# Performance work log

Measured on AMD Instinct MI355X. Metric: run time of the kernel, lower is better.

## Reference

```python
import jax, jax.numpy as jnp
import numpy as np

ALPHA = 0.25
GAMMA = 2.0
EPS = 1e-4

B, A, C, M = 4, 100000, 80, 32


def setup_inputs() -> dict:
    key = jax.random.key(0)
    k1, k2, k3, k4, k5, k6 = jax.random.split(key, 6)
    clsfs = jax.random.uniform(k1, (B, A, C), dtype=jnp.float32)
    rgrss = jax.random.normal(k2, (B, A, 4), dtype=jnp.float32)
    # anchors: random centers/sizes on a 512x512 image, converted to x1y1x2y2
    ctr = jax.random.uniform(k3, (A, 2), minval=32.0, maxval=480.0)
    wh = jax.random.uniform(k4, (A, 2), minval=16.0, maxval=256.0)
    anc = jnp.concatenate([ctr - 0.5 * wh, ctr + 0.5 * wh], axis=1)
    ancs = anc[None, :, :].astype(jnp.float32)
    # annotations: [x1,y1,x2,y2,label]; all valid labels in [0, C)
    gctr = jax.random.uniform(k5, (B, M, 2), minval=64.0, maxval=448.0)
    gwh = jax.random.uniform(k6, (B, M, 2), minval=24.0, maxval=200.0)
    lbl = jax.random.randint(jax.random.fold_in(key, 7), (B, M, 1), 0, C).astype(jnp.float32)
    annos = jnp.concatenate([gctr - 0.5 * gwh, gctr + 0.5 * gwh, lbl], axis=2).astype(jnp.float32)
    return {"clsfs": clsfs, "rgrss": rgrss, "ancs": ancs, "annos": annos}


def calc_iou(a, b):
    # a: [A,4], b: [M,4] -> [A,M]
    area_b = (b[:, 2] - b[:, 0]) * (b[:, 3] - b[:, 1])
    area_a = (a[:, 2] - a[:, 0]) * (a[:, 3] - a[:, 1])
    iw = jnp.clip(jnp.minimum(a[:, None, 2], b[None, :, 2]) - jnp.maximum(a[:, None, 0], b[None, :, 0]), 0.0)
    ih = jnp.clip(jnp.minimum(a[:, None, 3], b[None, :, 3]) - jnp.maximum(a[:, None, 1], b[None, :, 1]), 0.0)
    inter = iw * ih
    ua = jnp.clip(area_a[:, None] + area_b[None, :] - inter, 1e-8)
    return inter / ua


def _per_image(clsf, rgrs, anns, anc, ancw, anch, ancx, ancy):
    valid = anns[:, 4] != -1.0  # [M]
    has_anns = valid.any()
    ious = calc_iou(anc, anns[:, :4])  # [A,M]
    ious = jnp.where(valid[None, :], ious, -1.0)  # mask padded annotations
    maxiou = ious.max(axis=1)
    maxidx = ious.argmax(axis=1)
    assigned = anns[maxidx]  # [A,5]
    pos = maxiou >= 0.5
    posnum = pos.sum().astype(clsf.dtype)

    # classification targets: -1 ignore, 0 negative (<0.4), one-hot for pos
    clsf = jnp.clip(clsf, EPS, 1.0 - EPS)
    nc = clsf.shape[1]
    targets = jnp.full(clsf.shape, -1.0, dtype=clsf.dtype)
    targets = jnp.where((maxiou < 0.4)[:, None], 0.0, targets)
    onehot = jnp.arange(nc)[None, :] == assigned[:, 4].astype(jnp.int32)[:, None]
    targets = jnp.where(pos[:, None], jnp.where(onehot, 1.0, 0.0), targets)

    alpha = jnp.where(targets == 1.0, ALPHA, 1.0 - ALPHA)
    focal = alpha * jnp.where(targets == 1.0, 1.0 - clsf, clsf) ** GAMMA
    bce = -(targets * jnp.log(clsf) + (1.0 - targets) * jnp.log(1.0 - clsf))
    clsloss = jnp.where(targets != -1.0, focal * bce, 0.0).sum() / jnp.maximum(posnum, 1.0)

    gtw0 = assigned[:, 2] - assigned[:, 0]
    gth0 = assigned[:, 3] - assigned[:, 1]
    gtx = assigned[:, 0] + 0.5 * gtw0
    gty = assigned[:, 1] + 0.5 * gth0
    gtw = jnp.maximum(gtw0, 1.0)
    gth = jnp.maximum(gth0, 1.0)
    t = jnp.stack([(gtx - ancx) / ancw,
                   (gty - ancy) / anch,
                   jnp.log(gtw / ancw),
                   jnp.log(gth / anch)], axis=1)
    t = t / jnp.array([0.1, 0.1, 0.2, 0.2], dtype=clsf.dtype)
    diff = jnp.abs(t - rgrs)
    sl1 = jnp.where(diff <= 1.0 / 9.0, 0.5 * 9.0 * diff * diff, diff - 0.5 / 9.0)
    regloss = jnp.where(pos[:, None], sl1, 0.0).sum() / jnp.maximum(posnum * 4.0, 1.0)
    regloss = jnp.where(posnum > 0, regloss, 0.0)

    clsloss = jnp.where(has_anns, clsloss, 0.0)
    regloss = jnp.where(has_anns, regloss, 0.0)
    return clsloss, regloss


def reference(clsfs, rgrss, ancs, annos):
    anc = ancs[0]
    ancw = anc[:, 2] - anc[:, 0]
    anch = anc[:, 3] - anc[:, 1]
    ancx = anc[:, 0] + 0.5 * ancw
    ancy = anc[:, 1] + 0.5 * anch
    cls_l, reg_l = jax.vmap(_per_image, in_axes=(0, 0, 0, None, None, None, None, None))(
        clsfs, rgrss, annos, anc, ancw, anch, ancx, ancy)
    return cls_l.mean(keepdims=True), reg_l.mean(keepdims=True)
```

## Files before the change

kernel.cpp:

```cpp
#include <hip/hip_runtime.h>

#define F_EPS 1e-4f

constexpr int B = 4, A = 100000, C = 80, M = 32;
constexpr int APB = 256;
constexpr int THREADS = 256;
constexpr int VPA = C / 4;
constexpr int BPI = (A + APB - 1) / APB;
constexpr int FPT = APB * VPA / THREADS;

struct Part { float cls, reg, pos, pad; };

__device__ __forceinline__ float fterm(float p) {
  p = fminf(fmaxf(p, F_EPS), 1.0f - F_EPS);
  return p * p * (-__logf(1.0f - p));
}
__device__ __forceinline__ float fquad(float4 v) {
  return (fterm(v.x) + fterm(v.y)) + (fterm(v.z) + fterm(v.w));
}

__global__ __launch_bounds__(THREADS) void focal_main(
    const float* __restrict__ clsfs,
    const float* __restrict__ rgrss,
    const float* __restrict__ ancs,
    const float* __restrict__ annos,
    Part* __restrict__ part) {
  const int b = blockIdx.x / BPI;
  const int ablk = blockIdx.x - b * BPI;
  const int a0 = ablk * APB;
  const int tid = threadIdx.x;

  __shared__ float s_ann[M * 5];
  __shared__ float s_w[APB];
  __shared__ float s_red[3][THREADS / 64];

  if (tid < M * 5) s_ann[tid] = annos[b * M * 5 + tid];
  __syncthreads();

  float reg_acc = 0.0f, corr_acc = 0.0f, pos_acc = 0.0f;

  {
    const int a = a0 + tid;
    float wv = 0.0f;
    if (a < A) {
      const float4 anc = ((const float4*)ancs)[a];
      const float ax1 = anc.x, ay1 = anc.y, ax2 = anc.z, ay2 = anc.w;
      const float area_a = (ax2 - ax1) * (ay2 - ay1);
      float maxiou = -2.0f;
      int maxidx = 0;
      #pragma unroll
      for (int m = 0; m < M; ++m) {
        const float bx1 = s_ann[m * 5 + 0], by1 = s_ann[m * 5 + 1];
        const float bx2 = s_ann[m * 5 + 2], by2 = s_ann[m * 5 + 3];
        float iou = -1.0f;
        if (s_ann[m * 5 + 4] != -1.0f) {
          float iw = fmaxf(fminf(ax2, bx2) - fmaxf(ax1, bx1), 0.0f);
          float ih = fmaxf(fminf(ay2, by2) - fmaxf(ay1, by1), 0.0f);
          float inter = iw * ih;
          float area_b = (bx2 - bx1) * (by2 - by1);
          float ua = fmaxf(area_a + area_b - inter, 1e-8f);
          iou = inter / ua;
        }
        if (iou > maxiou) { maxiou = iou; maxidx = m; }
      }
      if (maxiou >= 0.5f) {
        const int lbl = (int)s_ann[maxidx * 5 + 4];
        pos_acc = 1.0f;
        wv = 1.0f;
        float p = clsfs[((size_t)b * A + a) * C + lbl];
        p = fminf(fmaxf(p, F_EPS), 1.0f - F_EPS);
        const float q = 1.0f - p;
        corr_acc = 0.25f * q * q * (-__logf(p)) - 0.75f * p * p * (-__logf(q));
        const float bx1 = s_ann[maxidx * 5 + 0], by1 = s_ann[maxidx * 5 + 1];
        const float bx2 = s_ann[maxidx * 5 + 2], by2 = s_ann[maxidx * 5 + 3];
        const float ancw = ax2 - ax1, anch = ay2 - ay1;
        const float ancx = ax1 + 0.5f * ancw, ancy = ay1 + 0.5f * anch;
        const float gtw0 = bx2 - bx1, gth0 = by2 - by1;
        const float gtx = bx1 + 0.5f * gtw0, gty = by1 + 0.5f * gth0;
        const float gtw = fmaxf(gtw0, 1.0f), gth = fmaxf(gth0, 1.0f);
        const float t0 = ((gtx - ancx) / ancw) / 0.1f;
        const float t1 = ((gty - ancy) / anch) / 0.1f;
        const float t2 = __logf(gtw / ancw) / 0.2f;
        const float t3 = __logf(gth / anch) / 0.2f;
        const float4 r = ((const float4*)rgrss)[(size_t)b * A + a];
        const float th = 1.0f / 9.0f, hh = 0.5f / 9.0f;
        float d;
        d = fabsf(t0 - r.x); reg_acc += (d <= th) ? 4.5f * d * d : d - hh;
        d = fabsf(t1 - r.y); reg_acc += (d <= th) ? 4.5f * d * d : d - hh;
        d = fabsf(t2 - r.z); reg_acc += (d <= th) ? 4.5f * d * d : d - hh;
        d = fabsf(t3 - r.w); reg_acc += (d <= th) ? 4.5f * d * d : d - hh;
      } else if (maxiou < 0.4f) {
        wv = 1.0f;
      }
    }
    s_w[tid] = wv;
  }
  __syncthreads();

  const int nanch = min(APB, A - a0);
  const float4* __restrict__ base4 =
      (const float4*)(clsfs + ((size_t)b * A + a0) * C);
  float acc0 = 0.f, acc1 = 0.f, acc2 = 0.f, acc3 = 0.f;
  if (nanch == APB) {
    #pragma unroll
    for (int k = 0; k < FPT; k += 4) {
      const int i0 = tid + (k + 0) * THREADS;
      const int i1 = tid + (k + 1) * THREADS;
      const int i2 = tid + (k + 2) * THREADS;
      const int i3 = tid + (k + 3) * THREADS;
      const float4 v0 = base4[i0];
      const float4 v1 = base4[i1];
      const float4 v2 = base4[i2];
      const float4 v3 = base4[i3];
      const float w0 = s_w[i0 / VPA];
      const float w1 = s_w[i1 / VPA];
      const float w2 = s_w[i2 / VPA];
      const float w3 = s_w[i3 / VPA];
      acc0 += w0 * fquad(v0);
      acc1 += w1 * fquad(v1);
      acc2 += w2 * fquad(v2);
      acc3 += w3 * fquad(v3);
    }
  } else {
    const int nvec = nanch * VPA;
    for (int i = tid; i < nvec; i += THREADS)
      acc0 += s_w[i / VPA] * fquad(base4[i]);
  }
  float cls_acc = 0.75f * ((acc0 + acc1) + (acc2 + acc3)) + corr_acc;

  float reg_f = reg_acc, pos_f = pos_acc;
  #pragma unroll
  for (int off = 32; off > 0; off >>= 1) {
    cls_acc += __shfl_down(cls_acc, off);
    reg_f   += __shfl_down(reg_f, off);
    pos_f   += __shfl_down(pos_f, off);
  }
  const int wave = tid >> 6, lane = tid & 63;
  if (lane == 0) { s_red[0][wave] = cls_acc; s_red[1][wave] = reg_f; s_red[2][wave] = pos_f; }
  __syncthreads();
  if (tid == 0) {
    float bc = 0.f, br = 0.f, bp = 0.f;
    #pragma unroll
    for (int v = 0; v < THREADS / 64; ++v) {
      bc += s_red[0][v]; br += s_red[1][v]; bp += s_red[2][v];
    }
    Part q; q.cls = bc; q.reg = br; q.pos = bp; q.pad = 0.f;
    part[blockIdx.x] = q;
  }
}

__global__ __launch_bounds__(256) void focal_final(
    const float* __restrict__ annos,
    const Part* __restrict__ part,
    float* __restrict__ out) {
  const int tid = threadIdx.x;
  const int wv = tid >> 6, lane = tid & 63;
  __shared__ float s_cls[4], s_reg[4];

  double c = 0.0, r = 0.0;
  float p = 0.f;
  for (int j = lane; j < BPI; j += 64) {
    const Part q = part[wv * BPI + j];
    c += (double)q.cls; r += (double)q.reg; p += q.pos;
  }
  #pragma unroll
  for (int off = 32; off > 0; off >>= 1) {
    c += __shfl_down(c, off);
    r += __shfl_down(r, off);
    p += __shfl_down(p, off);
  }
  const bool valid = (lane < M) && (annos[(wv * M + lane) * 5 + 4] != -1.0f);
  const bool has = __any(valid);
  if (lane == 0) {
    const float pn = p;
    float cls = (float)(c / (double)fmaxf(pn, 1.0f));
    float reg = (pn > 0.f) ? (float)(r / ((double)pn * 4.0)) : 0.0f;
    if (!has) { cls = 0.f; reg = 0.f; }
    s_cls[wv] = cls; s_reg[wv] = reg;
  }
  __syncthreads();
  if (tid == 0) {
    out[0] = (s_cls[0] + s_cls[1] + s_cls[2] + s_cls[3]) * 0.25f;
    out[1] = (s_reg[0] + s_reg[1] + s_reg[2] + s_reg[3]) * 0.25f;
  }
}

extern "C" void kernel_launch(void* const* d_in, const int* in_sizes, int n_in,
                              void* d_out, int out_size, void* d_ws, size_t ws_size,
                              hipStream_t stream) {
  const float* clsfs = (const float*)d_in[0];
  const float* rgrss = (const float*)d_in[1];
  const float* ancs  = (const float*)d_in[2];
  const float* annos = (const float*)d_in[3];
  float* out = (float*)d_out;
  Part* part = (Part*)d_ws;

  focal_main<<<dim3(B * BPI), dim3(THREADS), 0, stream>>>(
      clsfs, rgrss, ancs, annos, part);
  focal_final<<<1, 256, 0, stream>>>(annos, part, out);
}
```

Baseline: 42.45 us.

## Split anchor assignment and classification streaming into separate kernels

Anchor IoU matching now runs in its own kernel, which writes per-anchor negative weights to workspace. A separate grid-strided streaming kernel (512 blocks per image, 15-16 float4 loads per thread) reads the class scores. It uses log2 with the ln2 and 0.75 factors folded into the weight constant. This decouples the compute-heavy IoU phase from the bandwidth-bound sweep so the sweep can keep more loads in flight, at the cost of an extra launch and a weight-array round trip through memory.

```diff
diff --git a/kernel.cpp b/kernel.cpp
--- a/kernel.cpp
+++ b/kernel.cpp
@@ -3,155 +3,201 @@
 #define F_EPS 1e-4f
 
 constexpr int B = 4, A = 100000, C = 80, M = 32;
+constexpr int THREADS = 256;
 constexpr int APB = 256;
-constexpr int THREADS = 256;
+constexpr int BPI = (A + APB - 1) / APB;
 constexpr int VPA = C / 4;
-constexpr int BPI = (A + APB - 1) / APB;
-constexpr int FPT = APB * VPA / THREADS;
+constexpr int TVI = A * VPA;
+constexpr int SBX = 512;
+constexpr int SG = SBX * THREADS;
+constexpr float WNEG = -0.5198603854199589f;
 
 struct Part { float cls, reg, pos, pad; };
 
-__device__ __forceinline__ float fterm(float p) {
-  p = fminf(fmaxf(p, F_EPS), 1.0f - F_EPS);
-  return p * p * (-__logf(1.0f - p));
-}
-__device__ __forceinline__ float fquad(float4 v) {
-  return (fterm(v.x) + fterm(v.y)) + (fterm(v.z) + fterm(v.w));
-}
-
-__global__ __launch_bounds__(THREADS) void focal_main(
+__global__ __launch_bounds__(THREADS) void focal_assign(
     const float* __restrict__ clsfs,
     const float* __restrict__ rgrss,
     const float* __restrict__ ancs,
     const float* __restrict__ annos,
+    float* __restrict__ wn,
     Part* __restrict__ part) {
   const int b = blockIdx.x / BPI;
-  const int ablk = blockIdx.x - b * BPI;
-  const int a0 = ablk * APB;
+  const int a = (blockIdx.x - b * BPI) * APB + threadIdx.x;
   const int tid = threadIdx.x;
 
   __shared__ float s_ann[M * 5];
-  __shared__ float s_w[APB];
   __shared__ float s_red[3][THREADS / 64];
-
   if (tid < M * 5) s_ann[tid] = annos[b * M * 5 + tid];
   __syncthreads();
 
   float reg_acc = 0.0f, corr_acc = 0.0f, pos_acc = 0.0f;
 
-  {
-    const int a = a0 + tid;
+  if (a < A) {
     float wv = 0.0f;
-    if (a < A) {
-      const float4 anc = ((const float4*)ancs)[a];
-      const float ax1 = anc.x, ay1 = anc.y, ax2 = anc.z, ay2 = anc.w;
-      const float area_a = (ax2 - ax1) * (ay2 - ay1);
-      float maxiou = -2.0f;
-      int maxidx = 0;
-      #pragma unroll
-      for (int m = 0; m < M; ++m) {
-        const float bx1 = s_ann[m * 5 + 0], by1 = s_ann[m * 5 + 1];
-        const float bx2 = s_ann[m * 5 + 2], by2 = s_ann[m * 5 + 3];
-        float iou = -1.0f;
-        if (s_ann[m * 5 + 4] != -1.0f) {
-          float iw = fmaxf(fminf(ax2, bx2) - fmaxf(ax1, bx1), 0.0f);
-          float ih = fmaxf(fminf(ay2, by2) - fmaxf(ay1, by1), 0.0f);
-          float inter = iw * ih;
-          float area_b = (bx2 - bx1) * (by2 - by1);
-          float ua = fmaxf(area_a + area_b - inter, 1e-8f);
-          iou = inter / ua;
-        }
-        if (iou > maxiou) { maxiou = iou; maxidx = m; }
+    const float4 anc = ((const float4*)ancs)[a];
+    const float ax1 = anc.x, ay1 = anc.y, ax2 = anc.z, ay2 = anc.w;
+    const float area_a = (ax2 - ax1) * (ay2 - ay1);
+    float maxiou = -2.0f;
+    int maxidx = 0;
+    #pragma unroll
+    for (int m = 0; m < M; ++m) {
+      const float bx1 = s_ann[m * 5 + 0], by1 = s_ann[m * 5 + 1];
+      const float bx2 = s_ann[m * 5 + 2], by2 = s_ann[m * 5 + 3];
+      float iou = -1.0f;
+      if (s_ann[m * 5 + 4] != -1.0f) {
+        float iw = fmaxf(fminf(ax2, bx2) - fmaxf(ax1, bx1), 0.0f);
+        float ih = fmaxf(fminf(ay2, by2) - fmaxf(ay1, by1), 0.0f);
+        float inter = iw * ih;
+        float area_b = (bx2 - bx1) * (by2 - by1);
+        float ua = fmaxf(area_a + area_b - inter, 1e-8f);
+        iou = inter / ua;
       }
-      if (maxiou >= 0.5f) {
-        const int lbl = (int)s_ann[maxidx * 5 + 4];
-        pos_acc = 1.0f;
-        wv = 1.0f;
-        float p = clsfs[((size_t)b * A + a) * C + lbl];
-        p = fminf(fmaxf(p, F_EPS), 1.0f - F_EPS);
-        const float q = 1.0f - p;
-        corr_acc = 0.25f * q * q * (-__logf(p)) - 0.75f * p * p * (-__logf(q));
-        const float bx1 = s_ann[maxidx * 5 + 0], by1 = s_ann[maxidx * 5 + 1];
-        const float bx2 = s_ann[maxidx * 5 + 2], by2 = s_ann[maxidx * 5 + 3];
-        const float ancw = ax2 - ax1, anch = ay2 - ay1;
-        const float ancx = ax1 + 0.5f * ancw, ancy = ay1 + 0.5f * anch;
-        const float gtw0 = bx2 - bx1, gth0 = by2 - by1;
-        const float gtx = bx1 + 0.5f * gtw0, gty = by1 + 0.5f * gth0;
-        const float gtw = fmaxf(gtw0, 1.0f), gth = fmaxf(gth0, 1.0f);
-        const float t0 = ((gtx - ancx) / ancw) / 0.1f;
-        const float t1 = ((gty - ancy) / anch) / 0.1f;
-        const float t2 = __logf(gtw / ancw) / 0.2f;
-        const float t3 = __logf(gth / anch) / 0.2f;
-        const float4 r = ((const float4*)rgrss)[(size_t)b * A + a];
-        const float th = 1.0f / 9.0f, hh = 0.5f / 9.0f;
-        float d;
-        d = fabsf(t0 - r.x); reg_acc += (d <= th) ? 4.5f * d * d : d - hh;
-        d = fabsf(t1 - r.y); reg_acc += (d <= th) ? 4.5f * d * d : d - hh;
-        d = fabsf(t2 - r.z); reg_acc += (d <= th) ? 4.5f * d * d : d - hh;
-        d = fabsf(t3 - r.w); reg_acc += (d <= th) ? 4.5f * d * d : d - hh;
-      } else if (maxiou < 0.4f) {
-        wv = 1.0f;
-      }
+      if (iou > maxiou) { maxiou = iou; maxidx = m; }
     }
-    s_w[tid] = wv;
-  }
-  __syncthreads();
-
-  const int nanch = min(APB, A - a0);
-  const float4* __restrict__ base4 =
-      (const float4*)(clsfs + ((size_t)b * A + a0) * C);
-  float acc0 = 0.f, acc1 = 0.f, acc2 = 0.f, acc3 = 0.f;
-  if (nanch == APB) {
-    #pragma unroll
-    for (int k = 0; k < FPT; k += 4) {
-      const int i0 = tid + (k + 0) * THREADS;
-      const int i1 = tid + (k + 1) * THREADS;
-      const int i2 = tid + (k + 2) * THREADS;
-      const int i3 = tid + (k + 3) * THREADS;
-      const float4 v0 = base4[i0];
-      const float4 v1 = base4[i1];
-      const float4 v2 = base4[i2];
-      const float4 v3 = base4[i3];
-      const float w0 = s_w[i0 / VPA];
-      const float w1 = s_w[i1 / VPA];
-      const float w2 = s_w[i2 / VPA];
-      const float w3 = s_w[i3 / VPA];
-      acc0 += w0 * fquad(v0);
-      acc1 += w1 * fquad(v1);
-      acc2 += w2 * fquad(v2);
-      acc3 += w3 * fquad(v3);
+    if (maxiou >= 0.5f) {
+      const int lbl = (int)s_ann[maxidx * 5 + 4];
+      pos_acc = 1.0f;
+      wv = 1.0f;
+      float p = clsfs[((size_t)b * A + a) * C + lbl];
+      p = fminf(fmaxf(p, F_EPS), 1.0f - F_EPS);
+      const float q = 1.0f - p;
+      corr_acc = 0.25f * q * q * (-__logf(p)) - 0.75f * p * p * (-__logf(q));
+      const float bx1 = s_ann[maxidx * 5 + 0], by1 = s_ann[maxidx * 5 + 1];
+      const float bx2 = s_ann[maxidx * 5 + 2], by2 = s_ann[maxidx * 5 + 3];
+      const float ancw = ax2 - ax1, anch = ay2 - ay1;
+      const float ancx = ax1 + 0.5f * ancw, ancy = ay1 + 0.5f * anch;
+      const float gtw0 = bx2 - bx1, gth0 = by2 - by1;
+      const float gtx = bx1 + 0.5f * gtw0, gty = by1 + 0.5f * gth0;
+      const float gtw = fmaxf(gtw0, 1.0f), gth = fmaxf(gth0, 1.0f);
+      const float t0 = ((gtx - ancx) / ancw) / 0.1f;
+      const float t1 = ((gty - ancy) / anch) / 0.1f;
+      const float t2 = __logf(gtw / ancw) / 0.2f;
+      const float t3 = __logf(gth / anch) / 0.2f;
+      const float4 r = ((const float4*)rgrss)[(size_t)b * A + a];
+      const float th = 1.0f / 9.0f, hh = 0.5f / 9.0f;
+      float d;
+      d = fabsf(t0 - r.x); reg_acc += (d <= th) ? 4.5f * d * d : d - hh;
+      d = fabsf(t1 - r.y); reg_acc += (d <= th) ? 4.5f * d * d : d - hh;
+      d = fabsf(t2 - r.z); reg_acc += (d <= th) ? 4.5f * d * d : d - hh;
+      d = fabsf(t3 - r.w); reg_acc += (d <= th) ? 4.5f * d * d : d - hh;
+    } else if (maxiou < 0.4f) {
+      wv = 1.0f;
     }
-  } else {
-    const int nvec = nanch * VPA;
-    for (int i = tid; i < nvec; i += THREADS)
-      acc0 += s_w[i / VPA] * fquad(base4[i]);
-  }
-  float cls_acc = 0.75f * ((acc0 + acc1) + (acc2 + acc3)) + corr_acc;
-
-  float reg_f = reg_acc, pos_f = pos_acc;
+    wn[(size_t)b * A + a] = wv * WNEG;
+  }
+
+  float cls_f = corr_acc, reg_f = reg_acc, pos_f = pos_acc;
   #pragma unroll
   for (int off = 32; off > 0; off >>= 1) {
-    cls_acc += __shfl_down(cls_acc, off);
-    reg_f   += __shfl_down(reg_f, off);
-    pos_f   += __shfl_down(pos_f, off);
+    cls_f += __shfl_down(cls_f, off);
+    reg_f += __shfl_down(reg_f, off);
+    pos_f += __shfl_down(pos_f, off);
   }
   const int wave = tid >> 6, lane = tid & 63;
-  if (lane == 0) { s_red[0][wave] = cls_acc; s_red[1][wave] = reg_f; s_red[2][wave] = pos_f; }
+  if (lane == 0) { s_red[0][wave] = cls_f; s_red[1][wave] = reg_f; s_red[2][wave] = pos_f; }
   __syncthreads();
   if (tid == 0) {
     float bc = 0.f, br = 0.f, bp = 0.f;
     #pragma unroll
-    for (int v = 0; v < THREADS / 64; ++v) {
-      bc += s_red[0][v]; br += s_red[1][v]; bp += s_red[2][v];
-    }
+    for (int v = 0; v < THREADS / 64; ++v) { bc += s_red[0][v]; br += s_red[1][v]; bp += s_red[2][v]; }
     Part q; q.cls = bc; q.reg = br; q.pos = bp; q.pad = 0.f;
     part[blockIdx.x] = q;
+  }
+}
+
+__device__ __forceinline__ float gterm(float p) {
+  const float pc = fminf(fmaxf(p, F_EPS), 1.0f - F_EPS);
+  return pc * pc * __log2f(1.0f - pc);
+}
+__device__ __forceinline__ float gquad(float4 v) {
+  return (gterm(v.x) + gterm(v.y)) + (gterm(v.z) + gterm(v.w));
+}
+
+__global__ __launch_bounds__(THREADS) void focal_stream(
+    const float* __restrict__ clsfs,
+    const float* __restrict__ wn,
+    float* __restrict__ part2) {
+  const int b = blockIdx.y;
+  const float4* __restrict__ base = (const float4*)(clsfs + (size_t)b * A * C);
+  const float* __restrict__ w = wn + (size_t)b * A;
+  const int i0 = blockIdx.x * THREADS + threadIdx.x;
+
+  float a0 = 0.f, a1 = 0.f, a2 = 0.f, a3 = 0.f;
+
+  {
+    float4 v0 = base[i0];
+    float4 v1 = base[i0 + 1 * SG];
+    float4 v2 = base[i0 + 2 * SG];
+    float4 v3 = base[i0 + 3 * SG];
+    float4 v4 = base[i0 + 4 * SG];
+    float4 v5 = base[i0 + 5 * SG];
+    float4 v6 = base[i0 + 6 * SG];
+    float4 v7 = base[i0 + 7 * SG];
+    float w0 = w[(i0) / VPA];
+    float w1 = w[(i0 + 1 * SG) / VPA];
+    float w2 = w[(i0 + 2 * SG) / VPA];
+    float w3 = w[(i0 + 3 * SG) / VPA];
+    float w4 = w[(i0 + 4 * SG) / VPA];
+    float w5 = w[(i0 + 5 * SG) / VPA];
+    float w6 = w[(i0 + 6 * SG) / VPA];
+    float w7 = w[(i0 + 7 * SG) / VPA];
+    a0 += w0 * gquad(v0);
+    a1 += w1 * gquad(v1);
+    a2 += w2 * gquad(v2);
+    a3 += w3 * gquad(v3);
+    a0 += w4 * gquad(v4);
+    a1 += w5 * gquad(v5);
+    a2 += w6 * gquad(v6);
+    a3 += w7 * gquad(v7);
+  }
+  {
+    float4 v0 = base[i0 + 8 * SG];
+    float4 v1 = base[i0 + 9 * SG];
+    float4 v2 = base[i0 + 10 * SG];
+    float4 v3 = base[i0 + 11 * SG];
+    float4 v4 = base[i0 + 12 * SG];
+    float4 v5 = base[i0 + 13 * SG];
+    float4 v6 = base[i0 + 14 * SG];
+    float w0 = w[(i0 + 8 * SG) / VPA];
+    float w1 = w[(i0 + 9 * SG) / VPA];
+    float w2 = w[(i0 + 10 * SG) / VPA];
+    float w3 = w[(i0 + 11 * SG) / VPA];
+    float w4 = w[(i0 + 12 * SG) / VPA];
+    float w5 = w[(i0 + 13 * SG) / VPA];
+    float w6 = w[(i0 + 14 * SG) / VPA];
+    a0 += w0 * gquad(v0);
+    a1 += w1 * gquad(v1);
+    a2 += w2 * gquad(v2);
+    a3 += w3 * gquad(v3);
+    a0 += w4 * gquad(v4);
+    a1 += w5 * gquad(v5);
+    a2 += w6 * gquad(v6);
+  }
+  {
+    const int i = i0 + 15 * SG;
+    if (i < TVI) a3 += w[i / VPA] * gquad(base[i]);
+  }
+
+  float cls = (a0 + a1) + (a2 + a3);
+  #pragma unroll
+  for (int off = 32; off > 0; off >>= 1) cls += __shfl_down(cls, off);
+
+  __shared__ float s_red[THREADS / 64];
+  const int wave = threadIdx.x >> 6, lane = threadIdx.x & 63;
+  if (lane == 0) s_red[wave] = cls;
+  __syncthreads();
+  if (threadIdx.x == 0) {
+    float bc = 0.f;
+    #pragma unroll
+    for (int v = 0; v < THREADS / 64; ++v) bc += s_red[v];
+    part2[b * SBX + blockIdx.x] = bc;
   }
 }
 
 __global__ __launch_bounds__(256) void focal_final(
     const float* __restrict__ annos,
     const Part* __restrict__ part,
+    const float* __restrict__ part2,
     float* __restrict__ out) {
   const int tid = threadIdx.x;
   const int wv = tid >> 6, lane = tid & 63;
@@ -163,6 +209,7 @@
     const Part q = part[wv * BPI + j];
     c += (double)q.cls; r += (double)q.reg; p += q.pos;
   }
+  for (int j = lane; j < SBX; j += 64) c += (double)part2[wv * SBX + j];
   #pragma unroll
   for (int off = 32; off > 0; off >>= 1) {
     c += __shfl_down(c, off);
@@ -193,9 +240,13 @@
   const float* ancs  = (const float*)d_in[2];
   const float* annos = (const float*)d_in[3];
   float* out = (float*)d_out;
-  Part* part = (Part*)d_ws;
-
-  focal_main<<<dim3(B * BPI), dim3(THREADS), 0, stream>>>(
-      clsfs, rgrss, ancs, annos, part);
-  focal_final<<<1, 256, 0, stream>>>(annos, part, out);
-}
+
+  Part*  part  = (Part*)d_ws;
+  float* part2 = (float*)((char*)d_ws + 32768);
+  float* wn    = (float*)((char*)d_ws + 65536);
+
+  focal_assign<<<dim3(B * BPI), dim3(THREADS), 0, stream>>>(
+      clsfs, rgrss, ancs, annos, wn, part);
+  focal_stream<<<dim3(SBX, B), dim3(THREADS), 0, stream>>>(clsfs, wn, part2);
+  focal_final<<<1, 256, 0, stream>>>(annos, part, part2, out);
+}
```

Result: slower. 49.64 us (+16.9%).
